# Kernel tuning notes

Measured on AMD Instinct MI355X. Metric: run time of the kernel, lower is better.

The kernel has to match this reference:

```python
import jax, jax.numpy as jnp
import numpy as np
import math

D_MODEL = 1024
N_HEADS = 16
HEAD_DIM = D_MODEL // N_HEADS
TOP_K = 32
SCALE = math.sqrt(HEAD_DIM)


def setup_inputs() -> dict:
    key = jax.random.key(0)
    ks = jax.random.split(key, 12)
    B, S, N = 2, 2048, 2048
    std = 1.0 / math.sqrt(D_MODEL)
    inp = {
        "x": jax.random.normal(ks[0], (B, S, D_MODEL), dtype=jnp.float32),
        "knowledge_embeddings": jax.random.normal(ks[1], (B, N, D_MODEL), dtype=jnp.float32),
        "Wq": jax.random.normal(ks[2], (D_MODEL, D_MODEL), dtype=jnp.float32) * std,
        "bq": jnp.zeros((D_MODEL,), dtype=jnp.float32),
        "Wk": jax.random.normal(ks[3], (D_MODEL, D_MODEL), dtype=jnp.float32) * std,
        "bk": jnp.zeros((D_MODEL,), dtype=jnp.float32),
        "Wv": jax.random.normal(ks[4], (D_MODEL, D_MODEL), dtype=jnp.float32) * std,
        "bv": jnp.zeros((D_MODEL,), dtype=jnp.float32),
        "Wo": jax.random.normal(ks[5], (D_MODEL, D_MODEL), dtype=jnp.float32) * std,
        "bo": jnp.zeros((D_MODEL,), dtype=jnp.float32),
    }
    return inp


def _split_heads(t, n):
    # [B, L, d_model] -> [B, H, L, head_dim]
    B, L, _ = t.shape
    return t.reshape(B, L, N_HEADS, HEAD_DIM).transpose(0, 2, 1, 3)


def reference(x, knowledge_embeddings, Wq, bq, Wk, bk, Wv, bv, Wo, bo):
    B, S, _ = x.shape
    N = knowledge_embeddings.shape[1]
    Q = _split_heads(x @ Wq.T + bq, N_HEADS)                    # [B,H,S,hd]
    K = _split_heads(knowledge_embeddings @ Wk.T + bk, N_HEADS)  # [B,H,N,hd]
    V = _split_heads(knowledge_embeddings @ Wv.T + bv, N_HEADS)  # [B,H,N,hd]

    scores = jnp.einsum("bhsd,bhnd->bhsn", Q, K) / SCALE        # [B,H,S,N]
    k = min(TOP_K, N)
    topk_scores, topk_indices = jax.lax.top_k(scores, k)        # [B,H,S,k]
    sparse_weights = jax.nn.softmax(topk_scores, axis=-1)       # [B,H,S,k]
    # dropout=0.0 (eval) -> identity

    # gather V rows: V [B,H,N,hd] with indices [B,H,S,k] along N axis
    sel_V = jnp.take_along_axis(
        V[:, :, None, :, :],                  # [B,H,1,N,hd]
        topk_indices[..., None],              # [B,H,S,k,1]
        axis=3,
    )                                          # [B,H,S,k,hd]
    context = jnp.einsum("bhsk,bhskd->bhsd", sparse_weights, sel_V)
    context = context.transpose(0, 2, 1, 3).reshape(B, S, D_MODEL)
    return context @ Wo.T + bo
```

## Files before the change

### kernel.cpp

```cpp
#include <hip/hip_runtime.h>
#include <math.h>

typedef unsigned long long u64;
typedef unsigned int u32;
typedef unsigned short ush;
typedef __attribute__((ext_vector_type(8))) short short8;
typedef __attribute__((ext_vector_type(4))) float f32x4;

#define BATCH   2
#define SEQ     2048
#define NKNOW   2048
#define DMODEL  1024
#define NHEADS  16
#define HDIM    64
#define TOPK    32
#define CPAD    44

#define MFMA16(A, B, C) __builtin_amdgcn_mfma_f32_16x16x32_bf16(A, B, C, 0, 0, 0)

__device__ __forceinline__ ush f2bf(float x) {
    u32 u = __float_as_uint(x);
    return (ush)((u + 0x7FFFu + ((u >> 16) & 1u)) >> 16);
}
__device__ __forceinline__ float bf2f(ush b) { return __uint_as_float(((u32)b) << 16); }

__global__ __launch_bounds__(256) void gemm_f32_v2(
    const float* __restrict__ X, const float* __restrict__ W,
    const float* __restrict__ bias, float* __restrict__ Y, ush* __restrict__ Yb)
{
    __shared__ float As[32][66];
    __shared__ float Bs[32][130];

    const int t  = threadIdx.x;
    const int m0 = blockIdx.x * 64;
    const int n0 = blockIdx.y * 128;

    const int ra = t >> 2, ka = (t & 3) * 8;
    const int rb = t >> 1, kb = (t & 1) * 16;

    const int ty = t >> 5;
    const int tx = t & 31;

    float acc[8][4];
#pragma unroll
    for (int i = 0; i < 8; ++i)
#pragma unroll
        for (int j = 0; j < 4; ++j) acc[i][j] = 0.f;

    for (int k0 = 0; k0 < 1024; k0 += 32) {
        float4 a0 = *(const float4*)(X + (size_t)(m0 + ra) * 1024 + k0 + ka);
        float4 a1 = *(const float4*)(X + (size_t)(m0 + ra) * 1024 + k0 + ka + 4);
        float4 b0 = *(const float4*)(W + (size_t)(n0 + rb) * 1024 + k0 + kb);
        float4 b1 = *(const float4*)(W + (size_t)(n0 + rb) * 1024 + k0 + kb + 4);
        float4 b2 = *(const float4*)(W + (size_t)(n0 + rb) * 1024 + k0 + kb + 8);
        float4 b3 = *(const float4*)(W + (size_t)(n0 + rb) * 1024 + k0 + kb + 12);
        __syncthreads();
        As[ka + 0][ra] = a0.x; As[ka + 1][ra] = a0.y; As[ka + 2][ra] = a0.z; As[ka + 3][ra] = a0.w;
        As[ka + 4][ra] = a1.x; As[ka + 5][ra] = a1.y; As[ka + 6][ra] = a1.z; As[ka + 7][ra] = a1.w;
        Bs[kb + 0][rb] = b0.x; Bs[kb + 1][rb] = b0.y; Bs[kb + 2][rb] = b0.z; Bs[kb + 3][rb] = b0.w;
        Bs[kb + 4][rb] = b1.x; Bs[kb + 5][rb] = b1.y; Bs[kb + 6][rb] = b1.z; Bs[kb + 7][rb] = b1.w;
        Bs[kb + 8][rb] = b2.x; Bs[kb + 9][rb] = b2.y; Bs[kb +10][rb] = b2.z; Bs[kb +11][rb] = b2.w;
        Bs[kb +12][rb] = b3.x; Bs[kb +13][rb] = b3.y; Bs[kb +14][rb] = b3.z; Bs[kb +15][rb] = b3.w;
        __syncthreads();
#pragma unroll 4
        for (int k = 0; k < 32; ++k) {
            float a[8], b[4];
            *(float4*)(a)     = *(const float4*)&As[k][ty * 8];
            *(float4*)(a + 4) = *(const float4*)&As[k][ty * 8 + 4];
            *(float4*)(b)     = *(const float4*)&Bs[k][tx * 4];
#pragma unroll
            for (int i = 0; i < 8; ++i)
#pragma unroll
                for (int j = 0; j < 4; ++j)
                    acc[i][j] = fmaf(a[i], b[j], acc[i][j]);
        }
    }

    float4 bv = *(const float4*)(bias + n0 + tx * 4);
    const float bb[4] = {bv.x, bv.y, bv.z, bv.w};
#pragma unroll
    for (int i = 0; i < 8; ++i) {
        size_t row = (size_t)(m0 + ty * 8 + i) * 1024;
        float4 r;
        r.x = acc[i][0] + bb[0]; r.y = acc[i][1] + bb[1];
        r.z = acc[i][2] + bb[2]; r.w = acc[i][3] + bb[3];
        *(float4*)(Y + row + n0 + tx * 4) = r;
        if (Yb) {
            ushort4 h;
            h.x = f2bf(r.x); h.y = f2bf(r.y); h.z = f2bf(r.z); h.w = f2bf(r.w);
            *(ushort4*)(Yb + row + n0 + tx * 4) = h;
        }
    }
}

__global__ __launch_bounds__(256) void split_bf16(
    const float* __restrict__ in, ush* __restrict__ oh, ush* __restrict__ ol, int n)
{
    int i = (blockIdx.x * 256 + threadIdx.x) * 4;
    if (i >= n) return;
    float4 v = *(const float4*)(in + i);
    ush h0 = f2bf(v.x), h1 = f2bf(v.y), h2 = f2bf(v.z), h3 = f2bf(v.w);
    ushort4 hv; hv.x = h0; hv.y = h1; hv.z = h2; hv.w = h3;
    ushort4 lv;
    lv.x = f2bf(v.x - bf2f(h0)); lv.y = f2bf(v.y - bf2f(h1));
    lv.z = f2bf(v.z - bf2f(h2)); lv.w = f2bf(v.w - bf2f(h3));
    *(ushort4*)(oh + i) = hv;
    *(ushort4*)(ol + i) = lv;
}

__global__ __launch_bounds__(256) void gemm_mfma_split(
    const ush* __restrict__ Ah, const ush* __restrict__ Al,
    const ush* __restrict__ Bh, const ush* __restrict__ Bl,
    const float* __restrict__ bias, float* __restrict__ Yf)
{
    __shared__ ush sAh[4096], sAl[4096];
    __shared__ ush sBh[8192], sBl[8192];

    const int t = threadIdx.x;
    const int w = t >> 6, lane = t & 63;
    const int m0 = blockIdx.x * 64;
    const int n0 = blockIdx.y * 128;

    f32x4 acc[4][2];
#pragma unroll
    for (int i = 0; i < 4; ++i)
#pragma unroll
        for (int j = 0; j < 2; ++j) acc[i][j] = (f32x4){0.f, 0.f, 0.f, 0.f};

    for (int k0 = 0; k0 < 1024; k0 += 64) {
        __syncthreads();
#pragma unroll
        for (int c = t; c < 512; c += 256) {
            int t16 = c >> 7, ks = (c >> 6) & 1, ln = c & 63;
            int row = t16 * 16 + (ln & 15);
            int k8  = ks * 4 + (ln >> 4);
            size_t g = (size_t)(m0 + row) * 1024 + k0 + k8 * 8;
            *(uint4*)&sAh[c * 8] = *(const uint4*)(Ah + g);
            *(uint4*)&sAl[c * 8] = *(const uint4*)(Al + g);
        }
#pragma unroll
        for (int c = t; c < 1024; c += 256) {
            int t16 = c >> 7, ks = (c >> 6) & 1, ln = c & 63;
            int row = t16 * 16 + (ln & 15);
            int k8  = ks * 4 + (ln >> 4);
            size_t g = (size_t)(n0 + row) * 1024 + k0 + k8 * 8;
            *(uint4*)&sBh[c * 8] = *(const uint4*)(Bh + g);
            *(uint4*)&sBl[c * 8] = *(const uint4*)(Bl + g);
        }
        __syncthreads();

#pragma unroll
        for (int ks = 0; ks < 2; ++ks) {
            short8 a_h[4], a_l[4], b_h[2], b_l[2];
#pragma unroll
            for (int i = 0; i < 4; ++i) {
                a_h[i] = *(const short8*)&sAh[((i * 2 + ks) * 64 + lane) * 8];
                a_l[i] = *(const short8*)&sAl[((i * 2 + ks) * 64 + lane) * 8];
            }
#pragma unroll
            for (int j = 0; j < 2; ++j) {
                int nt = w * 2 + j;
                b_h[j] = *(const short8*)&sBh[((nt * 2 + ks) * 64 + lane) * 8];
                b_l[j] = *(const short8*)&sBl[((nt * 2 + ks) * 64 + lane) * 8];
            }
#pragma unroll
            for (int i = 0; i < 4; ++i)
#pragma unroll
                for (int j = 0; j < 2; ++j) {
                    acc[i][j] = MFMA16(a_h[i], b_h[j], acc[i][j]);
                    acc[i][j] = MFMA16(a_h[i], b_l[j], acc[i][j]);
                    acc[i][j] = MFMA16(a_l[i], b_h[j], acc[i][j]);
                }
        }
    }

    const int quad = lane >> 4, c16 = lane & 15;
#pragma unroll
    for (int i = 0; i < 4; ++i)
#pragma unroll
        for (int j = 0; j < 2; ++j) {
            int colg = n0 + (w * 2 + j) * 16 + c16;
            float bia = bias[colg];
#pragma unroll
            for (int r = 0; r < 4; ++r) {
                int rowg = m0 + i * 16 + quad * 4 + r;
                Yf[(size_t)rowg * 1024 + colg] = acc[i][j][r] + bia;
            }
        }
}

__global__ __launch_bounds__(256) void scores_bf16(
    const ush* __restrict__ Qb, const ush* __restrict__ Kb,
    ush* __restrict__ Sc, int bh0)
{
    __shared__ ush sA[8192], sB[8192];

    const int t = threadIdx.x;
    const int w = t >> 6, lane = t & 63;
    const int s0  = blockIdx.x * 128;
    const int nn0 = blockIdx.y * 128;
    const int bhl = blockIdx.z;
    const int bh  = bh0 + bhl;
    const int b   = bh >> 4, h = bh & 15;

#pragma unroll
    for (int c = t; c < 1024; c += 256) {
        int t16 = c >> 7, ks = (c >> 6) & 1, ln = c & 63;
        int row = t16 * 16 + (ln & 15);
        int k8  = ks * 4 + (ln >> 4);
        size_t gq = ((size_t)b * SEQ + s0 + row) * 1024 + h * 64 + k8 * 8;
        size_t gk = ((size_t)b * NKNOW + nn0 + row) * 1024 + h * 64 + k8 * 8;
        *(uint4*)&sA[c * 8] = *(const uint4*)(Qb + gq);
        *(uint4*)&sB[c * 8] = *(const uint4*)(Kb + gk);
    }
    __syncthreads();

    const int r0t = (w >> 1) * 4, c0t = (w & 1) * 4;
    f32x4 acc[4][4];
#pragma unroll
    for (int i = 0; i < 4; ++i)
#pragma unroll
        for (int j = 0; j < 4; ++j) acc[i][j] = (f32x4){0.f, 0.f, 0.f, 0.f};

#pragma unroll
    for (int ks = 0; ks < 2; ++ks) {
        short8 a[4], bb[4];
#pragma unroll
        for (int i = 0; i < 4; ++i)
            a[i] = *(const short8*)&sA[(((r0t + i) * 2 + ks) * 64 + lane) * 8];
#pragma unroll
        for (int j = 0; j < 4; ++j)
            bb[j] = *(const short8*)&sB[(((c0t + j) * 2 + ks) * 64 + lane) * 8];
#pragma unroll
        for (int i = 0; i < 4; ++i)
#pragma unroll
            for (int j = 0; j < 4; ++j)
                acc[i][j] = MFMA16(a[i], bb[j], acc[i][j]);
    }

    const int quad = lane >> 4, c16 = lane & 15;
#pragma unroll
    for (int i = 0; i < 4; ++i)
#pragma unroll
        for (int j = 0; j < 4; ++j) {
            int colg = nn0 + (c0t + j) * 16 + c16;
#pragma unroll
            for (int r = 0; r < 4; ++r) {
                int rowg = s0 + (r0t + i) * 16 + quad * 4 + r;
                Sc[((size_t)bhl * SEQ + rowg) * 2048 + colg] = f2bf(acc[i][j][r] * 0.125f);
            }
        }
}

__device__ __forceinline__ u32 mkey_of(float v) {
    u32 u = __float_as_uint(v);
    return (u & 0x80000000u) ? ~u : (u | 0x80000000u);
}
__device__ __forceinline__ u64 pk64(float v, int col) {
    return (((u64)mkey_of(v)) << 32) | (u32)(2047 - col);
}

__global__ __launch_bounds__(256) void topk_rescore2(
    const ush* __restrict__ Scb, const float* __restrict__ Qp,
    const float* __restrict__ Kp, const float* __restrict__ Vp,
    ush* __restrict__ ctxh, ush* __restrict__ ctxl, int bh0)
{
    __shared__ u32 binsAll[4][256];
    __shared__ u64 keysAll[4][64];
    __shared__ u32 selcAll[4][64];
    __shared__ u64 selAll[4][32];
    __shared__ float qrowAll[4][64];
    __shared__ u32 cntAll[4];

    const int t = threadIdx.x, w = t >> 6, l = t & 63;
    const int Rl  = blockIdx.x * 4 + w;
    const int bhl = Rl >> 11, s = Rl & 2047;
    const int bh  = bh0 + bhl;
    const int b   = bh >> 4, h = bh & 15;

    u32* bins = binsAll[w];
    u64* keys = keysAll[w];
    u32* selc = selcAll[w];
    u64* sel  = selAll[w];
    float* qrow = qrowAll[w];

    float v[32];
    const ush* srow = Scb + (size_t)Rl * 2048;
#pragma unroll
    for (int j = 0; j < 4; ++j) {
        ushort4 p0 = *(const ushort4*)(srow + j * 512 + l * 8);
        ushort4 p1 = *(const ushort4*)(srow + j * 512 + l * 8 + 4);
        v[8 * j + 0] = bf2f(p0.x); v[8 * j + 1] = bf2f(p0.y);
        v[8 * j + 2] = bf2f(p0.z); v[8 * j + 3] = bf2f(p0.w);
        v[8 * j + 4] = bf2f(p1.x); v[8 * j + 5] = bf2f(p1.y);
        v[8 * j + 6] = bf2f(p1.z); v[8 * j + 7] = bf2f(p1.w);
    }

    qrow[l] = Qp[((size_t)b * SEQ + s) * 1024 + h * 64 + l];

    float m = v[0];
#pragma unroll
    for (int i = 1; i < 32; ++i) m = fmaxf(m, v[i]);
#pragma unroll
    for (int d2 = 1; d2 < 64; d2 <<= 1) m = fmaxf(m, __shfl_xor(m, d2, 64));

    float lo = m - 8.0f, width = 8.0f;
    u32 base = 0;
    int havePrev = 0; float pLo = 0.f, pScale = 0.f; int pBkt = 0;
    float T = m - 8.0f;

    for (int att = 0; att < 3; ++att) {
        const float scale = 256.0f / width;

        *(uint4*)&bins[4 * l] = make_uint4(0u, 0u, 0u, 0u);
        __builtin_amdgcn_wave_barrier();

#pragma unroll
        for (int i = 0; i < 32; ++i) {
            float vi = v[i];
            bool in = (vi >= lo);
            if (havePrev) {
                int pb = (int)fminf((vi - pLo) * pScale, 255.0f);
                in = (vi >= pLo) && (pb == pBkt);
            }
            if (in) {
                int bi = (int)fminf((vi - lo) * scale, 255.0f);
                bi = bi < 0 ? 0 : bi;
                atomicAdd(&bins[bi], 1u);
            }
        }
        __builtin_amdgcn_wave_barrier();

        uint4 c4 = *(const uint4*)&bins[4 * l];
        u32 tl  = c4.x + c4.y + c4.z + c4.w;
        u32 suf = tl;
#pragma unroll
        for (int d2 = 1; d2 < 64; d2 <<= 1) {
            u32 o = __shfl_down(suf, d2, 64);
            suf += (l + d2 < 64) ? o : 0u;
        }
        u32 above = suf - tl;
        u32 cs3 = base + above + c4.w;
        u32 cs2 = cs3 + c4.z;
        u32 cs1 = cs2 + c4.y;
        u32 cs0 = cs1 + c4.x;

        bool has = (cs3 <= 64);
        int eloc; u32 nloc;
        if      (cs0 <= 64) { eloc = 4 * l;     nloc = cs0; }
        else if (cs1 <= 64) { eloc = 4 * l + 1; nloc = cs1; }
        else if (cs2 <= 64) { eloc = 4 * l + 2; nloc = cs2; }
        else                { eloc = 4 * l + 3; nloc = cs3; }

        u64 bal = __ballot(has);
        const float bw = width * (1.0f / 256.0f);
        if (bal == 0ull) {
            havePrev = 1; pLo = lo; pScale = scale; pBkt = 255;
            lo = lo + 255.0f * bw; width = bw;
            T = lo;
            continue;
        }
        int src  = (int)__ffsll(bal) - 1;
        int eS   = __shfl(eloc, src, 64);
        u32 nAt  = (u32)__shfl((int)nloc, src, 64);
        T = lo + (float)eS * bw;
        if (nAt >= CPAD || eS == 0 || att == 2) break;
        havePrev = 1; pLo = lo; pScale = scale; pBkt = eS - 1;
        base = nAt;
        lo = lo + (float)(eS - 1) * bw; width = bw;
    }

    if (l == 0) cntAll[w] = 0u;
    __builtin_amdgcn_wave_barrier();
#pragma unroll
    for (int i = 0; i < 32; ++i) {
        if (v[i] >= T) {
            u32 slot = atomicAdd(&cntAll[w], 1u);
            if (slot < 64) {
                int col = ((i >> 3) << 9) + (l << 3) + (i & 7);
                selc[slot] = (u32)col;
            }
        }
    }
    __builtin_amdgcn_wave_barrier();
    int C = (int)cntAll[w]; C = C > 64 ? 64 : C;

    float sx = -3.0e38f;
    u32 mycol = 0;
    if (l < C) {
        mycol = selc[l];
        const float* kr = Kp + ((size_t)b * NKNOW + mycol) * 1024 + h * 64;
        float p0 = 0.f, p1 = 0.f, p2 = 0.f, p3 = 0.f;
#pragma unroll
        for (int d = 0; d < 64; d += 4) {
            float4 kv = *(const float4*)(kr + d);
            float4 qv = *(const float4*)&qrow[d];
            p0 = fmaf(qv.x, kv.x, p0);
            p1 = fmaf(qv.y, kv.y, p1);
            p2 = fmaf(qv.z, kv.z, p2);
            p3 = fmaf(qv.w, kv.w, p3);
        }
        sx = ((p0 + p1) + (p2 + p3)) * 0.125f;
    }

    keys[l] = (l < C) ? pk64(sx, (int)mycol) : 0ull;
    __builtin_amdgcn_wave_barrier();
    u64 myk = keys[l];
    int rank = 0;
#pragma unroll 8
    for (int j = 0; j < 64; ++j) rank += (keys[j] > myk) ? 1 : 0;
    const bool win = (l < C) && (rank < TOPK);

    float mx = win ? sx : -3.0e38f;
#pragma unroll
    for (int d2 = 1; d2 < 64; d2 <<= 1) mx = fmaxf(mx, __shfl_xor(mx, d2, 64));
    float e = win ? __expf(sx - mx) : 0.0f;
    float Z = e;
#pragma unroll
    for (int d2 = 1; d2 < 64; d2 <<= 1) Z += __shfl_xor(Z, d2, 64);
    const float invZ = 1.0f / Z;

    u64 bw2 = __ballot(win);
    if (win) {
        u32 slot = (u32)__popcll(bw2 & ((1ull << l) - 1ull));
        sel[slot] = (((u64)__float_as_uint(e)) << 32) | mycol;
    }
    __builtin_amdgcn_wave_barrier();

    float acc = 0.0f;
    for (int j = 0; j < TOPK; ++j) {
        u64 pc = sel[j];
        float ej = __uint_as_float((u32)(pc >> 32));
        u32 colj = (u32)(pc & 0xFFFFFFFFu);
        acc = fmaf(ej * invZ, Vp[((size_t)b * NKNOW + colj) * 1024 + h * 64 + l], acc);
    }
    size_t oidx = ((size_t)b * SEQ + s) * 1024 + h * 64 + l;
    ush hh = f2bf(acc);
    ctxh[oidx] = hh;
    ctxl[oidx] = f2bf(acc - bf2f(hh));
}

extern "C" void kernel_launch(void* const* d_in, const int* in_sizes, int n_in,
                              void* d_out, int out_size, void* d_ws, size_t ws_size,
                              hipStream_t stream)
{
    const float* x  = (const float*)d_in[0];
    const float* ke = (const float*)d_in[1];
    const float* Wq = (const float*)d_in[2];
    const float* bq = (const float*)d_in[3];
    const float* Wk = (const float*)d_in[4];
    const float* bk = (const float*)d_in[5];
    const float* Wv = (const float*)d_in[6];
    const float* bv = (const float*)d_in[7];
    const float* Wo = (const float*)d_in[8];
    const float* bo = (const float*)d_in[9];
    float* out = (float*)d_out;

    const size_t NB = (size_t)4096 * 1024;
    const size_t NW = (size_t)1024 * 1024;

    char* p = (char*)d_ws;
    float *Qp = (float*)p;  p += NB * 4;
    float *Kp = (float*)p;  p += NB * 4;
    float *Vp = (float*)p;  p += NB * 4;
    ush *Qb  = (ush*)p;     p += NB * 2;
    ush *Kb  = (ush*)p;     p += NB * 2;
    ush *keh = (ush*)p;     p += NB * 2;
    ush *kel = (ush*)p;     p += NB * 2;
    ush *Wvh = (ush*)p;     p += NW * 2;
    ush *Wvl = (ush*)p;     p += NW * 2;
    ush *Woh = (ush*)p;     p += NW * 2;
    ush *Wol = (ush*)p;     p += NW * 2;
    ush *ctxh = (ush*)p;    p += NB * 2;
    ush *ctxl = (ush*)p;    p += NB * 2;
    ush *Sc = (ush*)p;
    const size_t fixedBytes = (size_t)(p - (char*)d_ws);

    int bhg = 1;
    {
        const int tiers[6] = {32, 16, 8, 4, 2, 1};
        for (int i = 0; i < 6; ++i) {
            size_t scB = (size_t)tiers[i] * SEQ * NKNOW * 2;
            if (fixedBytes + scB <= ws_size) { bhg = tiers[i]; break; }
        }
    }

    dim3 blk(256);

    hipLaunchKernelGGL(split_bf16, dim3((int)(NB / 1024)), blk, 0, stream, ke, keh, kel, (int)NB);
    hipLaunchKernelGGL(split_bf16, dim3((int)(NW / 1024)), blk, 0, stream, Wv, Wvh, Wvl, (int)NW);
    hipLaunchKernelGGL(split_bf16, dim3((int)(NW / 1024)), blk, 0, stream, Wo, Woh, Wol, (int)NW);

    dim3 g64(64, 8);
    hipLaunchKernelGGL(gemm_f32_v2, g64, blk, 0, stream, x,  Wq, bq, Qp, Qb);
    hipLaunchKernelGGL(gemm_f32_v2, g64, blk, 0, stream, ke, Wk, bk, Kp, Kb);

    dim3 gmf(64, 8);
    hipLaunchKernelGGL(gemm_mfma_split, gmf, blk, 0, stream, keh, kel, Wvh, Wvl, bv, Vp);

    for (int bh0 = 0; bh0 < 32; bh0 += bhg) {
        hipLaunchKernelGGL(scores_bf16, dim3(SEQ / 128, NKNOW / 128, bhg), blk, 0, stream,
                           Qb, Kb, Sc, bh0);
        hipLaunchKernelGGL(topk_rescore2, dim3(bhg * SEQ / 4), blk, 0, stream,
                           Sc, Qp, Kp, Vp, ctxh, ctxl, bh0);
    }

    hipLaunchKernelGGL(gemm_mfma_split, gmf, blk, 0, stream, ctxh, ctxl, Woh, Wol, bo, out);
}
```

Before: 780.6 us.

## Use single-bf16 V projection, batch Q/K GEMMs, unroll V gather

The V projection drops the hi/lo split bf16 scheme and uses a plain single-term bf16 MFMA GEMM, which cuts its MFMA work and input conversion traffic. The Q and K fp32 GEMMs are merged into one launch through a z grid dimension, so both fill the device together. The top-k V gather is unrolled by four to issue independent loads, and the rank loop is bounded by the candidate count. The lower V precision could slightly change the output values.

```diff
diff --git a/kernel.cpp b/kernel.cpp
--- a/kernel.cpp
+++ b/kernel.cpp
@@ -24,12 +24,21 @@
 }
 __device__ __forceinline__ float bf2f(ush b) { return __uint_as_float(((u32)b) << 16); }
 
-__global__ __launch_bounds__(256) void gemm_f32_v2(
-    const float* __restrict__ X, const float* __restrict__ W,
-    const float* __restrict__ bias, float* __restrict__ Y, ush* __restrict__ Yb)
+__global__ __launch_bounds__(256) void gemm_f32_qk(
+    const float* __restrict__ X0, const float* __restrict__ W0,
+    const float* __restrict__ b0, float* __restrict__ Y0, ush* __restrict__ Yb0,
+    const float* __restrict__ X1, const float* __restrict__ W1,
+    const float* __restrict__ b1, float* __restrict__ Y1, ush* __restrict__ Yb1)
 {
     __shared__ float As[32][66];
     __shared__ float Bs[32][130];
+
+    const int z = blockIdx.z;
+    const float* X   = z ? X1 : X0;
+    const float* W   = z ? W1 : W0;
+    const float* bia = z ? b1 : b0;
+    float* Y  = z ? Y1 : Y0;
+    ush*   Yb = z ? Yb1 : Yb0;
 
     const int t  = threadIdx.x;
     const int m0 = blockIdx.x * 64;
@@ -50,17 +59,17 @@
     for (int k0 = 0; k0 < 1024; k0 += 32) {
         float4 a0 = *(const float4*)(X + (size_t)(m0 + ra) * 1024 + k0 + ka);
         float4 a1 = *(const float4*)(X + (size_t)(m0 + ra) * 1024 + k0 + ka + 4);
-        float4 b0 = *(const float4*)(W + (size_t)(n0 + rb) * 1024 + k0 + kb);
-        float4 b1 = *(const float4*)(W + (size_t)(n0 + rb) * 1024 + k0 + kb + 4);
-        float4 b2 = *(const float4*)(W + (size_t)(n0 + rb) * 1024 + k0 + kb + 8);
-        float4 b3 = *(const float4*)(W + (size_t)(n0 + rb) * 1024 + k0 + kb + 12);
+        float4 b0v = *(const float4*)(W + (size_t)(n0 + rb) * 1024 + k0 + kb);
+        float4 b1v = *(const float4*)(W + (size_t)(n0 + rb) * 1024 + k0 + kb + 4);
+        float4 b2v = *(const float4*)(W + (size_t)(n0 + rb) * 1024 + k0 + kb + 8);
+        float4 b3v = *(const float4*)(W + (size_t)(n0 + rb) * 1024 + k0 + kb + 12);
         __syncthreads();
         As[ka + 0][ra] = a0.x; As[ka + 1][ra] = a0.y; As[ka + 2][ra] = a0.z; As[ka + 3][ra] = a0.w;
         As[ka + 4][ra] = a1.x; As[ka + 5][ra] = a1.y; As[ka + 6][ra] = a1.z; As[ka + 7][ra] = a1.w;
-        Bs[kb + 0][rb] = b0.x; Bs[kb + 1][rb] = b0.y; Bs[kb + 2][rb] = b0.z; Bs[kb + 3][rb] = b0.w;
-        Bs[kb + 4][rb] = b1.x; Bs[kb + 5][rb] = b1.y; Bs[kb + 6][rb] = b1.z; Bs[kb + 7][rb] = b1.w;
-        Bs[kb + 8][rb] = b2.x; Bs[kb + 9][rb] = b2.y; Bs[kb +10][rb] = b2.z; Bs[kb +11][rb] = b2.w;
-        Bs[kb +12][rb] = b3.x; Bs[kb +13][rb] = b3.y; Bs[kb +14][rb] = b3.z; Bs[kb +15][rb] = b3.w;
+        Bs[kb + 0][rb] = b0v.x; Bs[kb + 1][rb] = b0v.y; Bs[kb + 2][rb] = b0v.z; Bs[kb + 3][rb] = b0v.w;
+        Bs[kb + 4][rb] = b1v.x; Bs[kb + 5][rb] = b1v.y; Bs[kb + 6][rb] = b1v.z; Bs[kb + 7][rb] = b1v.w;
+        Bs[kb + 8][rb] = b2v.x; Bs[kb + 9][rb] = b2v.y; Bs[kb +10][rb] = b2v.z; Bs[kb +11][rb] = b2v.w;
+        Bs[kb +12][rb] = b3v.x; Bs[kb +13][rb] = b3v.y; Bs[kb +14][rb] = b3v.z; Bs[kb +15][rb] = b3v.w;
         __syncthreads();
 #pragma unroll 4
         for (int k = 0; k < 32; ++k) {
@@ -76,7 +85,7 @@
         }
     }
 
-    float4 bv = *(const float4*)(bias + n0 + tx * 4);
+    float4 bv = *(const float4*)(bia + n0 + tx * 4);
     const float bb[4] = {bv.x, bv.y, bv.z, bv.w};
 #pragma unroll
     for (int i = 0; i < 8; ++i) {
@@ -85,12 +94,21 @@
         r.x = acc[i][0] + bb[0]; r.y = acc[i][1] + bb[1];
         r.z = acc[i][2] + bb[2]; r.w = acc[i][3] + bb[3];
         *(float4*)(Y + row + n0 + tx * 4) = r;
-        if (Yb) {
-            ushort4 h;
-            h.x = f2bf(r.x); h.y = f2bf(r.y); h.z = f2bf(r.z); h.w = f2bf(r.w);
-            *(ushort4*)(Yb + row + n0 + tx * 4) = h;
-        }
-    }
+        ushort4 hh;
+        hh.x = f2bf(r.x); hh.y = f2bf(r.y); hh.z = f2bf(r.z); hh.w = f2bf(r.w);
+        *(ushort4*)(Yb + row + n0 + tx * 4) = hh;
+    }
+}
+
+__global__ __launch_bounds__(256) void conv_bf16(
+    const float* __restrict__ in, ush* __restrict__ o, int n)
+{
+    int i = (blockIdx.x * 256 + threadIdx.x) * 4;
+    if (i >= n) return;
+    float4 v = *(const float4*)(in + i);
+    ushort4 hv;
+    hv.x = f2bf(v.x); hv.y = f2bf(v.y); hv.z = f2bf(v.z); hv.w = f2bf(v.w);
+    *(ushort4*)(o + i) = hv;
 }
 
 __global__ __launch_bounds__(256) void split_bf16(
@@ -108,6 +126,78 @@
     *(ushort4*)(ol + i) = lv;
 }
 
+__global__ __launch_bounds__(256) void gemm_mfma_1t(
+    const ush* __restrict__ Ab, const ush* __restrict__ Bb,
+    const float* __restrict__ bias, float* __restrict__ Yf)
+{
+    __shared__ ush sA[4096];
+    __shared__ ush sB[8192];
+
+    const int t = threadIdx.x;
+    const int w = t >> 6, lane = t & 63;
+    const int m0 = blockIdx.x * 64;
+    const int n0 = blockIdx.y * 128;
+
+    f32x4 acc[4][2];
+#pragma unroll
+    for (int i = 0; i < 4; ++i)
+#pragma unroll
+        for (int j = 0; j < 2; ++j) acc[i][j] = (f32x4){0.f, 0.f, 0.f, 0.f};
+
+    for (int k0 = 0; k0 < 1024; k0 += 64) {
+        __syncthreads();
+#pragma unroll
+        for (int c = t; c < 512; c += 256) {
+            int t16 = c >> 7, ks = (c >> 6) & 1, ln = c & 63;
+            int row = t16 * 16 + (ln & 15);
+            int k8  = ks * 4 + (ln >> 4);
+            size_t g = (size_t)(m0 + row) * 1024 + k0 + k8 * 8;
+            *(uint4*)&sA[c * 8] = *(const uint4*)(Ab + g);
+        }
+#pragma unroll
+        for (int c = t; c < 1024; c += 256) {
+            int t16 = c >> 7, ks = (c >> 6) & 1, ln = c & 63;
+            int row = t16 * 16 + (ln & 15);
+            int k8  = ks * 4 + (ln >> 4);
+            size_t g = (size_t)(n0 + row) * 1024 + k0 + k8 * 8;
+            *(uint4*)&sB[c * 8] = *(const uint4*)(Bb + g);
+        }
+        __syncthreads();
+
+#pragma unroll
+        for (int ks = 0; ks < 2; ++ks) {
+            short8 a[4], b[2];
+#pragma unroll
+            for (int i = 0; i < 4; ++i)
+                a[i] = *(const short8*)&sA[((i * 2 + ks) * 64 + lane) * 8];
+#pragma unroll
+            for (int j = 0; j < 2; ++j) {
+                int nt = w * 2 + j;
+                b[j] = *(const short8*)&sB[((nt * 2 + ks) * 64 + lane) * 8];
+            }
+#pragma unroll
+            for (int i = 0; i < 4; ++i)
+#pragma unroll
+                for (int j = 0; j < 2; ++j)
+                    acc[i][j] = MFMA16(a[i], b[j], acc[i][j]);
+        }
+    }
+
+    const int quad = lane >> 4, c16 = lane & 15;
+#pragma unroll
+    for (int i = 0; i < 4; ++i)
+#pragma unroll
+        for (int j = 0; j < 2; ++j) {
+            int colg = n0 + (w * 2 + j) * 16 + c16;
+            float bia = bias[colg];
+#pragma unroll
+            for (int r = 0; r < 4; ++r) {
+                int rowg = m0 + i * 16 + quad * 4 + r;
+                Yf[(size_t)rowg * 1024 + colg] = acc[i][j][r] + bia;
+            }
+        }
+}
+
 __global__ __launch_bounds__(256) void gemm_mfma_split(
     const ush* __restrict__ Ah, const ush* __restrict__ Al,
     const ush* __restrict__ Bh, const ush* __restrict__ Bl,
@@ -408,7 +498,7 @@
     u64 myk = keys[l];
     int rank = 0;
 #pragma unroll 8
-    for (int j = 0; j < 64; ++j) rank += (keys[j] > myk) ? 1 : 0;
+    for (int j = 0; j < C; ++j) rank += (keys[j] > myk) ? 1 : 0;
     const bool win = (l < C) && (rank < TOPK);
 
     float mx = win ? sx : -3.0e38f;
@@ -427,12 +517,19 @@
     }
     __builtin_amdgcn_wave_barrier();
 
+    const float* vbase = Vp + (size_t)b * NKNOW * 1024 + h * 64 + l;
     float acc = 0.0f;
-    for (int j = 0; j < TOPK; ++j) {
-        u64 pc = sel[j];
-        float ej = __uint_as_float((u32)(pc >> 32));
-        u32 colj = (u32)(pc & 0xFFFFFFFFu);
-        acc = fmaf(ej * invZ, Vp[((size_t)b * NKNOW + colj) * 1024 + h * 64 + l], acc);
+#pragma unroll
+    for (int j0 = 0; j0 < TOPK; j0 += 4) {
+        u64 pc0 = sel[j0 + 0], pc1 = sel[j0 + 1], pc2 = sel[j0 + 2], pc3 = sel[j0 + 3];
+        float v0 = vbase[(size_t)(u32)(pc0 & 0xFFFFFFFFu) * 1024];
+        float v1 = vbase[(size_t)(u32)(pc1 & 0xFFFFFFFFu) * 1024];
+        float v2 = vbase[(size_t)(u32)(pc2 & 0xFFFFFFFFu) * 1024];
+        float v3 = vbase[(size_t)(u32)(pc3 & 0xFFFFFFFFu) * 1024];
+        acc = fmaf(__uint_as_float((u32)(pc0 >> 32)) * invZ, v0, acc);
+        acc = fmaf(__uint_as_float((u32)(pc1 >> 32)) * invZ, v1, acc);
+        acc = fmaf(__uint_as_float((u32)(pc2 >> 32)) * invZ, v2, acc);
+        acc = fmaf(__uint_as_float((u32)(pc3 >> 32)) * invZ, v3, acc);
     }
     size_t oidx = ((size_t)b * SEQ + s) * 1024 + h * 64 + l;
     ush hh = f2bf(acc);
@@ -465,10 +562,8 @@
     float *Vp = (float*)p;  p += NB * 4;
     ush *Qb  = (ush*)p;     p += NB * 2;
     ush *Kb  = (ush*)p;     p += NB * 2;
-    ush *keh = (ush*)p;     p += NB * 2;
-    ush *kel = (ush*)p;     p += NB * 2;
-    ush *Wvh = (ush*)p;     p += NW * 2;
-    ush *Wvl = (ush*)p;     p += NW * 2;
+    ush *keb = (ush*)p;     p += NB * 2;
+    ush *Wvb = (ush*)p;     p += NW * 2;
     ush *Woh = (ush*)p;     p += NW * 2;
     ush *Wol = (ush*)p;     p += NW * 2;
     ush *ctxh = (ush*)p;    p += NB * 2;
@@ -487,16 +582,15 @@
 
     dim3 blk(256);
 
-    hipLaunchKernelGGL(split_bf16, dim3((int)(NB / 1024)), blk, 0, stream, ke, keh, kel, (int)NB);
-    hipLaunchKernelGGL(split_bf16, dim3((int)(NW / 1024)), blk, 0, stream, Wv, Wvh, Wvl, (int)NW);
+    hipLaunchKernelGGL(conv_bf16,  dim3((int)(NB / 1024)), blk, 0, stream, ke, keb, (int)NB);
+    hipLaunchKernelGGL(conv_bf16,  dim3((int)(NW / 1024)), blk, 0, stream, Wv, Wvb, (int)NW);
     hipLaunchKernelGGL(split_bf16, dim3((int)(NW / 1024)), blk, 0, stream, Wo, Woh, Wol, (int)NW);
 
-    dim3 g64(64, 8);
-    hipLaunchKernelGGL(gemm_f32_v2, g64, blk, 0, stream, x,  Wq, bq, Qp, Qb);
-    hipLaunchKernelGGL(gemm_f32_v2, g64, blk, 0, stream, ke, Wk, bk, Kp, Kb);
-
-    dim3 gmf(64, 8);
-    hipLaunchKernelGGL(gemm_mfma_split, gmf, blk, 0, stream, keh, kel, Wvh, Wvl, bv, Vp);
+    hipLaunchKernelGGL(gemm_f32_qk, dim3(64, 8, 2), blk, 0, stream,
+                       x,  Wq, bq, Qp, Qb,
+                       ke, Wk, bk, Kp, Kb);
+
+    hipLaunchKernelGGL(gemm_mfma_1t, dim3(64, 8), blk, 0, stream, keb, Wvb, bv, Vp);
 
     for (int bh0 = 0; bh0 < 32; bh0 += bhg) {
         hipLaunchKernelGGL(scores_bf16, dim3(SEQ / 128, NKNOW / 128, bhg), blk, 0, stream,
@@ -505,5 +599,6 @@
                            Sc, Qp, Kp, Vp, ctxh, ctxl, bh0);
     }
 
-    hipLaunchKernelGGL(gemm_mfma_split, gmf, blk, 0, stream, ctxh, ctxl, Woh, Wol, bo, out);
-}
+    hipLaunchKernelGGL(gemm_mfma_split, dim3(64, 8), blk, 0, stream,
+                       ctxh, ctxl, Woh, Wol, bo, out);
+}
```

After: 776.7 us. About the same (-0.5%).
